# Optimization experiments

Measured on AMD Instinct MI355X. Metric: run time of the kernel, lower is better.

The kernel has to match this reference:

```python
import jax, jax.numpy as jnp
import numpy as np

B, S, H = 16, 4096, 512   # batch, seq frames, conv_dim[-1]
G, V, D = 2, 320, 256     # groups, codevectors per group, codevector_dim


def setup_inputs() -> dict:
    key = jax.random.key(0)
    k1, k2, k3 = jax.random.split(key, 3)
    hidden_states = jax.random.normal(k1, (B, S, H), dtype=jnp.float32)
    W = jax.random.normal(k2, (H, G * V), dtype=jnp.float32) * 0.02
    b = jnp.zeros((G * V,), dtype=jnp.float32)
    codevectors = jax.random.normal(k3, (1, G * V, D // G), dtype=jnp.float32)
    return {"hidden_states": hidden_states, "W": W, "b": b,
            "codevectors": codevectors, "num_groups": G}


def reference(hidden_states, W, b, codevectors, num_groups):
    Bb, Ss, Hh = hidden_states.shape
    GV = W.shape[1]
    g = num_groups
    v = GV // g
    d = codevectors.shape[-1]
    BT = Bb * Ss

    # weight_proj: [B,S,H] @ [H, G*V] -> logits per (token, group, var)
    logits = (hidden_states @ W + b).reshape(BT, g, v)

    # eval path: hard argmax one-hot over codevectors per group
    idx = jnp.argmax(logits, axis=-1)              # [BT, g] int

    # one-hot x codebook multiply-reduce == gather from codebook
    cb = codevectors.reshape(g, v, d)              # [g, v, d]
    gathered = cb[jnp.arange(g)[None, :], idx]     # [BT, g, d]
    out = gathered.reshape(Bb, Ss, g * d)          # [B, S, codevector_dim]

    # perplexity over one-hot probs: marginal = mean of one-hots = counts/BT
    marginal = jnp.zeros((g, v), dtype=jnp.float32)
    marginal = marginal.at[jnp.arange(g)[None, :], idx].add(1.0) / BT
    perplexity = jnp.exp(-jnp.sum(marginal * jnp.log(marginal + 1e-7), axis=-1)).sum()

    return out, perplexity
```

## Files before the change

kernel.cpp:

```cpp
#include <hip/hip_runtime.h>
#include <hip/hip_bf16.h>

constexpr int BT = 65536;
constexpr int K  = 512;
constexpr int V  = 320;
constexpr int G  = 2;
constexpr int Dg = 128;
constexpr int MT = 64;
constexpr int NSTEP = 8;
constexpr size_t WS_IMG = 4096;

using short8 = __attribute__((ext_vector_type(8))) short;
using f32x4  = __attribute__((ext_vector_type(4))) float;

static __device__ __forceinline__ unsigned short f2bf(float x) {
    unsigned u = __float_as_uint(x);
    unsigned r = 0x7FFFu + ((u >> 16) & 1u);
    return (unsigned short)((u + r) >> 16);
}
static __device__ __forceinline__ unsigned pk2(float a, float b) {
    return (unsigned)f2bf(a) | ((unsigned)f2bf(b) << 16);
}
static __device__ __forceinline__ f32x4 mfma16(short8 a, short8 b, f32x4 c) {
    return __builtin_amdgcn_mfma_f32_16x16x32_bf16(a, b, c, 0, 0, 0);
}

__global__ __launch_bounds__(256) void vq_prep(const float* __restrict__ Wm,
                                               unsigned char* __restrict__ img)
{
    int id   = blockIdx.x * 256 + threadIdx.x;
    int lane = id & 63;
    int s    = id >> 6;
    int nt   = s % 5;
    int wcq  = (s / 5) & 3;
    int tk   = s / 20;
    int g    = tk >> 4;
    int t    = tk & 15;
    int col  = g * V + wcq * 80 + nt * 16 + (lane & 15);
    int kb   = t * 32 + (lane >> 4) * 8;
    unsigned p[4];
#pragma unroll
    for (int jj = 0; jj < 4; ++jj)
        p[jj] = pk2(Wm[(size_t)(kb + 2 * jj) * 640 + col],
                    Wm[(size_t)(kb + 2 * jj + 1) * 640 + col]);
    *reinterpret_cast<uint4*>(img + (size_t)id * 16) = make_uint4(p[0], p[1], p[2], p[3]);
}

__global__ __launch_bounds__(512) void vq_main(
    const float* __restrict__ hs, const unsigned char* __restrict__ img,
    const float* __restrict__ bv, const float* __restrict__ cbv,
    float* __restrict__ out, unsigned int* __restrict__ hist)
{
    __shared__ __align__(16) unsigned char smem[49152];

    const int tid  = threadIdx.x;
    const int bid  = blockIdx.x;
    const int g    = (bid >> 3) & 1;
    const int rblk = (bid & 7) | ((bid >> 4) << 3);
    const int r0   = rblk * MT;
    const int w    = tid >> 6;
    const int lane = tid & 63;
    const int l4   = lane & 15;
    const int lc   = lane >> 4;
    const int wc   = w & 3;
    const int h    = w >> 2;

    f32x4 acc[2][5] = {};

    const int arow = tid >> 3, akq = tid & 7;
    const float* aptr = hs + (size_t)(r0 + arow) * K + akq * 8;
    const int awoff = (arow * 128 + akq * 16) ^ ((arow & 7) << 4);
    const int a_base = ((h * 32 + l4) * 128 + lc * 16) ^ ((l4 & 7) << 4);
    const unsigned char* bsrc = img + (size_t)g * 327680 + (size_t)tid * 16;
    const int b_rd = 8192 + wc * 5120 + lane * 16;

    auto packA = [&](float4 x, float4 y) {
        *reinterpret_cast<uint4*>(&smem[awoff]) =
            make_uint4(pk2(x.x, x.y), pk2(x.z, x.w), pk2(y.x, y.y), pk2(y.z, y.w));
    };

    float4 ax = *reinterpret_cast<const float4*>(aptr);
    float4 ay = *reinterpret_cast<const float4*>(aptr + 4);

    for (int s = 0; s < NSTEP; ++s) {
        const unsigned char* bs = bsrc + (size_t)s * 40960;
#pragma unroll
        for (int i = 0; i < 5; ++i)
            __builtin_amdgcn_global_load_lds(
                (const __attribute__((address_space(1))) void*)(bs + i * 8192),
                (__attribute__((address_space(3))) void*)(&smem[8192 + i * 8192 + tid * 16]),
                16, 0, 0);
        packA(ax, ay);
        __syncthreads();
        if (s + 1 < NSTEP) {
            ax = *reinterpret_cast<const float4*>(aptr + (s + 1) * 64);
            ay = *reinterpret_cast<const float4*>(aptr + (s + 1) * 64 + 4);
        }
        __builtin_amdgcn_s_setprio(1);
#pragma unroll
        for (int kk = 0; kk < 2; ++kk) {
            short8 av[2];
#pragma unroll
            for (int mt = 0; mt < 2; ++mt)
                av[mt] = *reinterpret_cast<const short8*>(
                    &smem[a_base + mt * 2048 + kk * 64]);
#pragma unroll
            for (int nt = 0; nt < 5; ++nt) {
                short8 bb = *reinterpret_cast<const short8*>(
                    &smem[b_rd + kk * 20480 + nt * 1024]);
                acc[0][nt] = mfma16(av[0], bb, acc[0][nt]);
                acc[1][nt] = mfma16(av[1], bb, acc[1][nt]);
            }
        }
        __builtin_amdgcn_s_setprio(0);
        __syncthreads();
    }

    float biasv[5];
#pragma unroll
    for (int nt = 0; nt < 5; ++nt) biasv[nt] = bv[g * V + wc * 80 + nt * 16 + l4];

    float* red_v = reinterpret_cast<float*>(smem);
    int*   red_i = reinterpret_cast<int*>(smem + 1024);
    int*   idx_s = reinterpret_cast<int*>(smem + 2048);

#pragma unroll
    for (int mt = 0; mt < 2; ++mt) {
#pragma unroll
        for (int reg = 0; reg < 4; ++reg) {
            float bestv = acc[mt][0][reg] + biasv[0];
            int   besti = wc * 80 + l4;
#pragma unroll
            for (int nt = 1; nt < 5; ++nt) {
                float v = acc[mt][nt][reg] + biasv[nt];
                int   ci = wc * 80 + nt * 16 + l4;
                if (v > bestv) { bestv = v; besti = ci; }
            }
#pragma unroll
            for (int m = 1; m < 16; m <<= 1) {
                float ov = __shfl_xor(bestv, m);
                int   oi = __shfl_xor(besti, m);
                if (ov > bestv || (ov == bestv && oi < besti)) { bestv = ov; besti = oi; }
            }
            if (l4 == 0) {
                int row = h * 32 + mt * 16 + lc * 4 + reg;
                red_v[row * 4 + wc] = bestv;
                red_i[row * 4 + wc] = besti;
            }
        }
    }
    __syncthreads();

    int my_bi = -1;
    if (tid < MT) {
        float bb = red_v[tid * 4]; int bi = red_i[tid * 4];
#pragma unroll
        for (int c = 1; c < 4; ++c) {
            float v = red_v[tid * 4 + c]; int ii = red_i[tid * 4 + c];
            if (v > bb || (v == bb && ii < bi)) { bb = v; bi = ii; }
        }
        idx_s[tid] = bi;
        my_bi = bi;
    }
    __syncthreads();

#pragma unroll
    for (int i = 0; i < 4; ++i) {
        int idx = i * 512 + tid;
        int row = idx >> 5;
        int d4  = idx & 31;
        int vi  = idx_s[row];
        float4 val = *reinterpret_cast<const float4*>(&cbv[((size_t)(g * V + vi)) * Dg + d4 * 4]);
        *reinterpret_cast<float4*>(&out[((size_t)(r0 + row)) * (G * Dg) + g * Dg + d4 * 4]) = val;
    }
    if (my_bi >= 0) atomicAdd(&hist[g * V + my_bi], 1u);
}

__global__ void vq_ppl(const unsigned int* __restrict__ hist, float* __restrict__ outp)
{
    int lane = threadIdx.x;
    float ppl = 0.0f;
    for (int g = 0; g < G; ++g) {
        float local = 0.0f;
        for (int v = lane; v < V; v += 64) {
            float m = (float)hist[g * V + v] * (1.0f / (float)BT);
            local += m * logf(m + 1e-7f);
        }
#pragma unroll
        for (int off = 32; off; off >>= 1) local += __shfl_down(local, off);
        if (lane == 0) ppl += expf(-local);
    }
    if (lane == 0) outp[0] = ppl;
}

extern "C" void kernel_launch(void* const* d_in, const int* in_sizes, int n_in,
                              void* d_out, int out_size, void* d_ws, size_t ws_size,
                              hipStream_t stream)
{
    const float* hs  = (const float*)d_in[0];
    const float* Wm  = (const float*)d_in[1];
    const float* bv  = (const float*)d_in[2];
    const float* cbv = (const float*)d_in[3];
    float* out = (float*)d_out;

    unsigned int*  hist = (unsigned int*)d_ws;
    unsigned char* img  = (unsigned char*)d_ws + WS_IMG;

    hipMemsetAsync(d_ws, 0, G * V * sizeof(unsigned int), stream);
    vq_prep<<<160, 256, 0, stream>>>(Wm, img);
    vq_main<<<2048, 512, 0, stream>>>(hs, img, bv, cbv, out, hist);
    vq_ppl<<<1, 64, 0, stream>>>(hist, out + (size_t)BT * G * Dg);
}
```

Measured before the change: 99.72 us.

## Switch projection GEMM from bf16 to fp8 e4m3 MFMA with rescaled weights

Converts both hidden states and the weight image to fp8 e4m3, with weights scaled by 16 and bias scaled to match, and uses the fp8 16x16x32 MFMA. This halves the weight-image size, the LDS footprint and the LDS traffic, and reorganises the shared-memory layouts for 8-byte operands. The aim is to cut memory and LDS bandwidth and shared-memory pressure. The cost is much lower precision in the logits, which can change argmax results on near ties and so change outputs compared with the fp32 reference.

```diff
diff --git a/kernel.cpp b/kernel.cpp
--- a/kernel.cpp
+++ b/kernel.cpp
@@ -1,5 +1,6 @@
 #include <hip/hip_runtime.h>
 #include <hip/hip_bf16.h>
+#include <hip/hip_fp8.h>
 
 constexpr int BT = 65536;
 constexpr int K  = 512;
@@ -10,19 +11,22 @@
 constexpr int NSTEP = 8;
 constexpr size_t WS_IMG = 4096;
 
-using short8 = __attribute__((ext_vector_type(8))) short;
-using f32x4  = __attribute__((ext_vector_type(4))) float;
-
-static __device__ __forceinline__ unsigned short f2bf(float x) {
-    unsigned u = __float_as_uint(x);
-    unsigned r = 0x7FFFu + ((u >> 16) & 1u);
-    return (unsigned short)((u + r) >> 16);
-}
-static __device__ __forceinline__ unsigned pk2(float a, float b) {
-    return (unsigned)f2bf(a) | ((unsigned)f2bf(b) << 16);
-}
-static __device__ __forceinline__ f32x4 mfma16(short8 a, short8 b, f32x4 c) {
-    return __builtin_amdgcn_mfma_f32_16x16x32_bf16(a, b, c, 0, 0, 0);
+using f32x4 = __attribute__((ext_vector_type(4))) float;
+
+static __device__ __forceinline__ unsigned cvt4(float a, float b, float c, float d) {
+#if __has_builtin(__builtin_amdgcn_cvt_pk_fp8_f32)
+    int r = 0;
+    r = __builtin_amdgcn_cvt_pk_fp8_f32(a, b, r, false);
+    r = __builtin_amdgcn_cvt_pk_fp8_f32(c, d, r, true);
+    return (unsigned)r;
+#else
+    __hip_fp8_e4m3 ha(a), hb(b), hc(c), hd(d);
+    return (unsigned)ha.__x | ((unsigned)hb.__x << 8) |
+           ((unsigned)hc.__x << 16) | ((unsigned)hd.__x << 24);
+#endif
+}
+static __device__ __forceinline__ f32x4 mfma_fp8(long long a, long long b, f32x4 c) {
+    return __builtin_amdgcn_mfma_f32_16x16x32_fp8_fp8(a, b, c, 0, 0, 0);
 }
 
 __global__ __launch_bounds__(256) void vq_prep(const float* __restrict__ Wm,
@@ -30,20 +34,19 @@
 {
     int id   = blockIdx.x * 256 + threadIdx.x;
     int lane = id & 63;
-    int s    = id >> 6;
-    int nt   = s % 5;
-    int wcq  = (s / 5) & 3;
-    int tk   = s / 20;
-    int g    = tk >> 4;
-    int t    = tk & 15;
-    int col  = g * V + wcq * 80 + nt * 16 + (lane & 15);
-    int kb   = t * 32 + (lane >> 4) * 8;
-    unsigned p[4];
-#pragma unroll
-    for (int jj = 0; jj < 4; ++jj)
-        p[jj] = pk2(Wm[(size_t)(kb + 2 * jj) * 640 + col],
-                    Wm[(size_t)(kb + 2 * jj + 1) * 640 + col]);
-    *reinterpret_cast<uint4*>(img + (size_t)id * 16) = make_uint4(p[0], p[1], p[2], p[3]);
+    int r    = id >> 6;
+    int nt   = r % 5;  r /= 5;
+    int wc   = r & 3;  r >>= 2;
+    int kk   = r & 1;  r >>= 1;
+    int s    = r & 7;
+    int g    = r >> 3;
+    int col  = g * V + wc * 80 + nt * 16 + (lane & 15);
+    int kb   = s * 64 + kk * 32 + (lane >> 4) * 8;
+    float v[8];
+#pragma unroll
+    for (int j = 0; j < 8; ++j) v[j] = 16.0f * Wm[(size_t)(kb + j) * 640 + col];
+    *reinterpret_cast<uint2*>(img + (size_t)id * 8) =
+        make_uint2(cvt4(v[0], v[1], v[2], v[3]), cvt4(v[4], v[5], v[6], v[7]));
 }
 
 __global__ __launch_bounds__(512) void vq_main(
@@ -51,7 +54,7 @@
     const float* __restrict__ bv, const float* __restrict__ cbv,
     float* __restrict__ out, unsigned int* __restrict__ hist)
 {
-    __shared__ __align__(16) unsigned char smem[49152];
+    __shared__ __align__(16) unsigned char smem[24576];
 
     const int tid  = threadIdx.x;
     const int bid  = blockIdx.x;
@@ -61,34 +64,40 @@
     const int w    = tid >> 6;
     const int lane = tid & 63;
     const int l4   = lane & 15;
-    const int lc   = lane >> 4;
     const int wc   = w & 3;
     const int h    = w >> 2;
+    const int lc   = lane >> 4;
+    (void)lc;
 
     f32x4 acc[2][5] = {};
 
     const int arow = tid >> 3, akq = tid & 7;
     const float* aptr = hs + (size_t)(r0 + arow) * K + akq * 8;
-    const int awoff = (arow * 128 + akq * 16) ^ ((arow & 7) << 4);
-    const int a_base = ((h * 32 + l4) * 128 + lc * 16) ^ ((l4 & 7) << 4);
-    const unsigned char* bsrc = img + (size_t)g * 327680 + (size_t)tid * 16;
-    const int b_rd = 8192 + wc * 5120 + lane * 16;
+    const int awoff = (((arow >> 5) * 2 + ((arow >> 4) & 1)) * 2 + (akq >> 2)) * 512
+                      + ((arow & 15) + 16 * (akq & 3)) * 8;
+    const unsigned char* bsrc = img + (size_t)g * 163840 + (size_t)tid * 16;
+    const int b_rd = 4096 + wc * 5 * 512 + lane * 8;
 
     auto packA = [&](float4 x, float4 y) {
-        *reinterpret_cast<uint4*>(&smem[awoff]) =
-            make_uint4(pk2(x.x, x.y), pk2(x.z, x.w), pk2(y.x, y.y), pk2(y.z, y.w));
+        *reinterpret_cast<uint2*>(&smem[awoff]) =
+            make_uint2(cvt4(x.x, x.y, x.z, x.w), cvt4(y.x, y.y, y.z, y.w));
     };
 
     float4 ax = *reinterpret_cast<const float4*>(aptr);
     float4 ay = *reinterpret_cast<const float4*>(aptr + 4);
 
     for (int s = 0; s < NSTEP; ++s) {
-        const unsigned char* bs = bsrc + (size_t)s * 40960;
-#pragma unroll
-        for (int i = 0; i < 5; ++i)
+        const unsigned char* bs = bsrc + (size_t)s * 20480;
+#pragma unroll
+        for (int i = 0; i < 2; ++i)
             __builtin_amdgcn_global_load_lds(
                 (const __attribute__((address_space(1))) void*)(bs + i * 8192),
-                (__attribute__((address_space(3))) void*)(&smem[8192 + i * 8192 + tid * 16]),
+                (__attribute__((address_space(3))) void*)(&smem[4096 + i * 8192 + tid * 16]),
+                16, 0, 0);
+        if (tid < 256)
+            __builtin_amdgcn_global_load_lds(
+                (const __attribute__((address_space(1))) void*)(bs + 16384),
+                (__attribute__((address_space(3))) void*)(&smem[4096 + 16384 + tid * 16]),
                 16, 0, 0);
         packA(ax, ay);
         __syncthreads();
@@ -99,17 +108,16 @@
         __builtin_amdgcn_s_setprio(1);
 #pragma unroll
         for (int kk = 0; kk < 2; ++kk) {
-            short8 av[2];
-#pragma unroll
-            for (int mt = 0; mt < 2; ++mt)
-                av[mt] = *reinterpret_cast<const short8*>(
-                    &smem[a_base + mt * 2048 + kk * 64]);
+            long long a0 = *reinterpret_cast<const long long*>(
+                &smem[((h * 2 + 0) * 2 + kk) * 512 + lane * 8]);
+            long long a1 = *reinterpret_cast<const long long*>(
+                &smem[((h * 2 + 1) * 2 + kk) * 512 + lane * 8]);
 #pragma unroll
             for (int nt = 0; nt < 5; ++nt) {
-                short8 bb = *reinterpret_cast<const short8*>(
-                    &smem[b_rd + kk * 20480 + nt * 1024]);
-                acc[0][nt] = mfma16(av[0], bb, acc[0][nt]);
-                acc[1][nt] = mfma16(av[1], bb, acc[1][nt]);
+                long long bb = *reinterpret_cast<const long long*>(
+                    &smem[b_rd + kk * 10240 + nt * 512]);
+                acc[0][nt] = mfma_fp8(a0, bb, acc[0][nt]);
+                acc[1][nt] = mfma_fp8(a1, bb, acc[1][nt]);
             }
         }
         __builtin_amdgcn_s_setprio(0);
@@ -118,7 +126,7 @@
 
     float biasv[5];
 #pragma unroll
-    for (int nt = 0; nt < 5; ++nt) biasv[nt] = bv[g * V + wc * 80 + nt * 16 + l4];
+    for (int nt = 0; nt < 5; ++nt) biasv[nt] = 16.0f * bv[g * V + wc * 80 + nt * 16 + l4];
 
     float* red_v = reinterpret_cast<float*>(smem);
     int*   red_i = reinterpret_cast<int*>(smem + 1024);
@@ -143,7 +151,7 @@
                 if (ov > bestv || (ov == bestv && oi < besti)) { bestv = ov; besti = oi; }
             }
             if (l4 == 0) {
-                int row = h * 32 + mt * 16 + lc * 4 + reg;
+                int row = h * 32 + mt * 16 + (lane >> 4) * 4 + reg;
                 red_v[row * 4 + wc] = bestv;
                 red_i[row * 4 + wc] = besti;
             }
```

New measurement: 91.02 us. 8.7% less time.
